# Performance work log

Measured on AMD Instinct MI355X. Metric: run time of the kernel, lower is better.

## Reference

```python
import jax, jax.numpy as jnp
import numpy as np

N, E, DIN, H, CHID, COUT, S = 20000, 320000, 128, 4, 64, 64, 32
EPS_BN = 1e-5


def setup_inputs() -> dict:
    key = jax.random.key(0)
    ks = jax.random.split(key, 20)
    g = lambda k, shp, s=0.1: jax.random.normal(k, shp, dtype=jnp.float32) * s
    return {
        "x": jax.random.normal(ks[0], (N, DIN), dtype=jnp.float32),
        "edge_index": jax.random.randint(ks[1], (2, E), 0, N, dtype=jnp.int32),
        "struct_feat": jax.random.normal(ks[2], (N, S), dtype=jnp.float32),
        # GATConv (layer 1)
        "W1": g(ks[3], (H * CHID, DIN)),
        "att_src1": g(ks[4], (1, H, CHID)),
        "att_dst1": g(ks[5], (1, H, CHID)),
        "bias1": jnp.zeros((CHID,), jnp.float32),
        # HybridGateGATLayer (layer 2)
        "W2": g(ks[6], (H * COUT, CHID)),
        "att_src2": g(ks[7], (1, H, COUT)),
        "att_dst2": g(ks[8], (1, H, COUT)),
        "bias2": jnp.zeros((COUT,), jnp.float32),
        "Wt": g(ks[9], (1, S)),
        "bt": jnp.zeros((1,), jnp.float32),
        "We1": g(ks[10], (8, 4), 0.5),
        "be1": jnp.zeros((8,), jnp.float32),
        "We2": g(ks[11], (1, 8), 0.5),
        "be2": jnp.zeros((1,), jnp.float32),
        "betas": jnp.array([1.15, 0.85, 0.1, 0.08, 0.12], jnp.float32),
    }


def _seg_softmax(logits, seg, n):
    m = jax.ops.segment_max(logits, seg, num_segments=n)
    m = jnp.where(jnp.isfinite(m), m, 0.0)
    ex = jnp.exp(logits - m[seg])
    s = jax.ops.segment_sum(ex, seg, num_segments=n)
    return ex / (s[seg] + 1e-16)


def _cos(a, b):
    na = jnp.maximum(jnp.linalg.norm(a, axis=-1), 1e-8)
    nb = jnp.maximum(jnp.linalg.norm(b, axis=-1), 1e-8)
    return (a * b).sum(-1) / (na * nb)


def reference(x, edge_index, struct_feat, W1, att_src1, att_dst1, bias1,
              W2, att_src2, att_dst2, bias2, Wt, bt, We1, be1, We2, be2, betas):
    n = x.shape[0]
    src0, dst0 = edge_index[0], edge_index[1]
    # ---- layer 1: standard GATConv with self loops, concat=False (head mean) ----
    loop = jnp.arange(n, dtype=src0.dtype)
    src = jnp.concatenate([src0, loop])
    dst = jnp.concatenate([dst0, loop])
    h = (x @ W1.T).reshape(n, H, CHID)
    a_s = (h * att_src1).sum(-1)  # [N,H]
    a_d = (h * att_dst1).sum(-1)
    al = jax.nn.leaky_relu(a_s[src] + a_d[dst], 0.2)  # [E+N,H]
    alpha1 = _seg_softmax(al, dst, n)
    out1 = jax.ops.segment_sum(h[src] * alpha1[..., None], dst, num_segments=n)
    h1 = jax.nn.relu(out1.mean(1) + bias1)  # [N,CHID]
    # batch norm (affine=False, batch stats, biased var)
    mu = h1.mean(0)
    var = ((h1 - mu) ** 2).mean(0)
    h1 = (h1 - mu) / jnp.sqrt(var + EPS_BN)
    # ---- layer 2: HybridGateGATLayer (no self loops) ----
    x2 = (h1 @ W2.T).reshape(n, H, COUT)
    node_trust = jax.nn.sigmoid(struct_feat @ Wt.T + bt).squeeze(-1)  # [N]
    as2 = (x2 * att_src2).sum(-1)
    ad2 = (x2 * att_dst2).sum(-1)
    j, i = src0, dst0
    alpha_raw = jax.nn.leaky_relu(as2[j] + ad2[i], 0.2)  # [E,H]
    struct_sim = _cos(struct_feat[j], struct_feat[i])  # [E]
    xf = x2.reshape(n, H * COUT)
    feat_sim = _cos(xf[j], xf[i])
    agreement = struct_sim * feat_sim
    conflict = jnp.abs(struct_sim - feat_sim)
    cues = jnp.stack([struct_sim, feat_sim, agreement, conflict], axis=-1)  # [E,4]
    gate = (jax.nn.relu(cues @ We1.T + be1) @ We2.T + be2).squeeze(-1)
    edge_bonus = jax.nn.sigmoid(gate) * jax.nn.relu(agreement)
    edge_trust = jnp.sqrt(jnp.clip(node_trust[j] * node_trust[i], 0.0))
    trust_bonus = edge_trust * jax.nn.relu(0.5 * (struct_sim + feat_sim))
    gate_logit = (betas[0] * struct_sim + betas[1] * feat_sim + betas[2] * agreement
                  + betas[3] * edge_bonus + betas[4] * trust_bonus)
    alpha2 = _seg_softmax(alpha_raw + gate_logit[:, None], i, n)  # [E,H]
    out2 = jax.ops.segment_sum(x2[j] * alpha2[..., None], i, num_segments=n)
    return out2.mean(1) + bias2  # [N,COUT]
```

## Files before the change

### kernel.cpp

```cpp
#include <hip/hip_runtime.h>
#include <hip/hip_bf16.h>
#include <hip/hip_fp16.h>

#define C_DIN 128
#define C_H 4
#define C_CH 64
#define C_HC 256
#define C_S 32
#define ACH 32
#define MBLK 64
#define XROW 264

typedef __attribute__((ext_vector_type(8))) _Float16 half8;
typedef __attribute__((ext_vector_type(4))) float f32x4;

__device__ __forceinline__ float lrelu(float x) { return x >= 0.f ? x : 0.2f * x; }

__device__ __forceinline__ float sub_sum32(float v) {
#pragma unroll
    for (int off = 16; off > 0; off >>= 1) v += __shfl_xor(v, off);
    return v;
}

__global__ void k_count(const int* __restrict__ dst, int* __restrict__ deg, int E) {
    int e = blockIdx.x * blockDim.x + threadIdx.x;
    if (e < E) atomicAdd(&deg[dst[e]], 1);
}

__global__ void k_scan(const int* __restrict__ deg, int* __restrict__ row_ptr,
                       int* __restrict__ cursor, int n) {
    __shared__ int part[1024];
    int t = threadIdx.x;
    const int C = (n + 1023) / 1024;
    int base = t * C;
    int s = 0;
    for (int k = 0; k < C; ++k) {
        int idx = base + k;
        if (idx < n) s += deg[idx];
    }
    part[t] = s;
    __syncthreads();
    for (int off = 1; off < 1024; off <<= 1) {
        int v = (t >= off) ? part[t - off] : 0;
        __syncthreads();
        part[t] += v;
        __syncthreads();
    }
    int run = (t == 0) ? 0 : part[t - 1];
    for (int k = 0; k < C; ++k) {
        int idx = base + k;
        if (idx < n) { row_ptr[idx] = run; cursor[idx] = run; run += deg[idx]; }
    }
    if (t == 1023) row_ptr[n] = run;
}

__global__ void k_scatter(const int* __restrict__ src, const int* __restrict__ dst,
                          int* __restrict__ cursor, int* __restrict__ adj_src, int E) {
    int e = blockIdx.x * blockDim.x + threadIdx.x;
    if (e < E) {
        int d = dst[e];
        int p = atomicAdd(&cursor[d], 1);
        adj_src[p] = src[e];
    }
}

__global__ void k_prepw(const float* __restrict__ W1, const float* __restrict__ W2,
                        _Float16* __restrict__ W1f, _Float16* __restrict__ W2f) {
    int i = blockIdx.x * blockDim.x + threadIdx.x;
    if (i < 4096) {
        int ks = i >> 10, rem = i & 1023, nt = rem >> 6, lpos = rem & 63;
        int c = nt * 16 + (lpos & 15);
        int kb = (ks * 4 + (lpos >> 4)) * 8;
        const float4* src = (const float4*)(W1 + (size_t)c * C_DIN + kb);
        float4 f0 = src[0], f1 = src[1];
        _Float16* dst = &W1f[(size_t)i * 8];
        dst[0] = (_Float16)f0.x; dst[1] = (_Float16)f0.y;
        dst[2] = (_Float16)f0.z; dst[3] = (_Float16)f0.w;
        dst[4] = (_Float16)f1.x; dst[5] = (_Float16)f1.y;
        dst[6] = (_Float16)f1.z; dst[7] = (_Float16)f1.w;
    } else if (i < 4096 + 2048) {
        int ii = i - 4096;
        int ks = ii >> 10, rem = ii & 1023, nt = rem >> 6, lpos = rem & 63;
        int c = nt * 16 + (lpos & 15);
        int kb = (ks * 4 + (lpos >> 4)) * 8;
        const float4* src = (const float4*)(W2 + (size_t)c * C_CH + kb);
        float4 f0 = src[0], f1 = src[1];
        _Float16* dst = &W2f[(size_t)ii * 8];
        dst[0] = (_Float16)f0.x; dst[1] = (_Float16)f0.y;
        dst[2] = (_Float16)f0.z; dst[3] = (_Float16)f0.w;
        dst[4] = (_Float16)f1.x; dst[5] = (_Float16)f1.y;
        dst[6] = (_Float16)f1.z; dst[7] = (_Float16)f1.w;
    }
}

__global__ __launch_bounds__(256) void k_gemm1(
    const float* __restrict__ x, const _Float16* __restrict__ W1f,
    const float* __restrict__ att_s, const float* __restrict__ att_d,
    __half* __restrict__ hh_out, float* __restrict__ a_s, float* __restrict__ a_d, int n) {
    __shared__ __align__(16) _Float16 as_[4 * 4 * 64 * 8];
    int t = threadIdx.x;
    int r0 = blockIdx.x * MBLK;
    {
        int row = t >> 2, q = t & 3;
        int rr = r0 + row;
        int mt = row >> 4, rl = row & 15;
        const float4* xrow = (const float4*)(x + (size_t)rr * C_DIN);
#pragma unroll
        for (int cc = 0; cc < 4; ++cc) {
            int ch = q * 4 + cc;
            float4 f0 = make_float4(0, 0, 0, 0), f1 = make_float4(0, 0, 0, 0);
            if (rr < n) { f0 = xrow[ch * 2]; f1 = xrow[ch * 2 + 1]; }
            int ks = ch >> 2, lg = ch & 3;
            _Float16* dst = &as_[(((ks * 4 + mt) * 64) + (lg * 16 + rl)) * 8];
            dst[0] = (_Float16)f0.x; dst[1] = (_Float16)f0.y;
            dst[2] = (_Float16)f0.z; dst[3] = (_Float16)f0.w;
            dst[4] = (_Float16)f1.x; dst[5] = (_Float16)f1.y;
            dst[6] = (_Float16)f1.z; dst[7] = (_Float16)f1.w;
        }
    }
    __syncthreads();
    int w = t >> 6, l = t & 63;
    const half8* Wv = (const half8*)W1f;
    f32x4 acc[4][4];
#pragma unroll
    for (int mt = 0; mt < 4; ++mt)
#pragma unroll
        for (int nt = 0; nt < 4; ++nt) acc[mt][nt] = (f32x4){0.f, 0.f, 0.f, 0.f};
#pragma unroll
    for (int ks = 0; ks < 4; ++ks) {
        half8 af[4], bf[4];
#pragma unroll
        for (int mt = 0; mt < 4; ++mt)
            af[mt] = *(const half8*)&as_[(((ks * 4 + mt) * 64) + l) * 8];
#pragma unroll
        for (int nt = 0; nt < 4; ++nt)
            bf[nt] = Wv[((ks * 16 + (w * 4 + nt)) * 64) + l];
#pragma unroll
        for (int mt = 0; mt < 4; ++mt)
#pragma unroll
            for (int nt = 0; nt < 4; ++nt)
                acc[mt][nt] = __builtin_amdgcn_mfma_f32_16x16x32_f16(af[mt], bf[nt],
                                                                     acc[mt][nt], 0, 0, 0);
    }
    int cl = l & 15, rg = l >> 4;
    float atv_s[4], atv_d[4];
#pragma unroll
    for (int nt = 0; nt < 4; ++nt) {
        atv_s[nt] = att_s[w * 64 + nt * 16 + cl];
        atv_d[nt] = att_d[w * 64 + nt * 16 + cl];
    }
#pragma unroll
    for (int mt = 0; mt < 4; ++mt) {
#pragma unroll
        for (int r = 0; r < 4; ++r) {
            int rr = r0 + mt * 16 + rg * 4 + r;
            float vs = 0.f, vd = 0.f;
#pragma unroll
            for (int nt = 0; nt < 4; ++nt) {
                float v = acc[mt][nt][r];
                vs += atv_s[nt] * v;
                vd += atv_d[nt] * v;
                if (rr < n)
                    hh_out[(size_t)rr * C_HC + w * 64 + nt * 16 + cl] = __float2half(v);
            }
#pragma unroll
            for (int off = 1; off < 16; off <<= 1) {
                vs += __shfl_xor(vs, off);
                vd += __shfl_xor(vd, off);
            }
            if (cl == 0 && rr < n) { a_s[rr * C_H + w] = vs; a_d[rr * C_H + w] = vd; }
        }
    }
}

__global__ void k_layer1(const int* __restrict__ row_ptr, const int* __restrict__ adj_src,
                         const __half* __restrict__ hhlf, const float* __restrict__ a_s,
                         const float* __restrict__ a_d, const float* __restrict__ bias1,
                         float* __restrict__ h1) {
    int d = blockIdx.x;
    int t = threadIdx.x, hh = t >> 5, cp = t & 31;
    int beg = row_ptr[d], end = row_ptr[d + 1];
    float adh = a_d[d * C_H + hh];
    float p_self = expf(lrelu(a_s[d * C_H + hh] + adh));
    __shared__ float alpha_l[C_H][ACH];
    __shared__ int src_l[ACH];
    const __half2* selfrow = (const __half2*)(hhlf + (size_t)d * C_HC + hh * 64);
    float2 sv = __half22float2(selfrow[cp]);
    float accx = p_self * sv.x, accy = p_self * sv.y;
    float s_part = (cp == 0) ? p_self : 0.f;
    for (int cbeg = beg; cbeg < end; cbeg += ACH) {
        int cn = min(end - cbeg, ACH);
        __syncthreads();
        if (cp < cn) {
            int s = adj_src[cbeg + cp];
            if (hh == 0) src_l[cp] = s;
            float p = expf(lrelu(a_s[s * C_H + hh] + adh));
            alpha_l[hh][cp] = p;
            s_part += p;
        }
        __syncthreads();
        for (int i = 0; i < cn; ++i) {
            int s = src_l[i];
            float a = alpha_l[hh][i];
            float2 v = __half22float2(
                *(const __half2*)(hhlf + (size_t)s * C_HC + hh * 64 + cp * 2));
            accx += a * v.x;
            accy += a * v.y;
        }
    }
    float s = sub_sum32(s_part);
    float inv = 1.f / (s + 1e-16f);
    __shared__ float2 red[128];
    red[t] = make_float2(accx * inv, accy * inv);
    __syncthreads();
    if (t < 32) {
        float2 r0 = red[t], r1 = red[t + 32], r2 = red[t + 64], r3 = red[t + 96];
        float2 b = *(const float2*)&bias1[t * 2];
        float vx = (r0.x + r1.x + r2.x + r3.x) * 0.25f + b.x;
        float vy = (r0.y + r1.y + r2.y + r3.y) * 0.25f + b.y;
        *(float2*)&h1[(size_t)d * C_CH + t * 2] =
            make_float2(fmaxf(vx, 0.f), fmaxf(vy, 0.f));
    }
}

__global__ void k_bnstats(const float* __restrict__ h1, float* __restrict__ bn, int n) {
    int t = threadIdx.x;
    int c = t & 63, rg = t >> 6;
    float s = 0.f, s2 = 0.f;
    for (int r = blockIdx.x * 4 + rg; r < n; r += gridDim.x * 4) {
        float v = h1[(size_t)r * C_CH + c];
        s += v;
        s2 += v * v;
    }
    __shared__ float ls[256], ls2[256];
    ls[t] = s; ls2[t] = s2;
    __syncthreads();
    if (t < 64) {
        s = ls[t] + ls[t + 64] + ls[t + 128] + ls[t + 192];
        s2 = ls2[t] + ls2[t + 64] + ls2[t + 128] + ls2[t + 192];
        atomicAdd(&bn[c], s);
        atomicAdd(&bn[64 + c], s2);
    }
}

__global__ __launch_bounds__(256) void k_gemm2(
    const float* __restrict__ h1, const _Float16* __restrict__ W2f,
    const float* __restrict__ att_s, const float* __restrict__ att_d,
    const float* __restrict__ bn, __half* __restrict__ x2h,
    float* __restrict__ as2, float* __restrict__ ad2, float* __restrict__ nf, int n) {
    __shared__ __align__(16) _Float16 as_[2 * 4 * 64 * 8];
    __shared__ float nq[64][4];
    int t = threadIdx.x;
    int r0 = blockIdx.x * MBLK;
    {
        int row = t >> 2, q = t & 3;
        int rr = r0 + row;
        int mt = row >> 4, rl = row & 15;
        const float invN = 1.f / (float)n;
        const float4* hrow = (const float4*)(h1 + (size_t)rr * C_CH);
#pragma unroll
        for (int cc = 0; cc < 2; ++cc) {
            int ch = q * 2 + cc;
            float4 f0 = make_float4(0, 0, 0, 0), f1 = make_float4(0, 0, 0, 0);
            if (rr < n) { f0 = hrow[ch * 2]; f1 = hrow[ch * 2 + 1]; }
            float4 s0 = *(const float4*)&bn[ch * 8];
            float4 s1 = *(const float4*)&bn[ch * 8 + 4];
            float4 q0 = *(const float4*)&bn[64 + ch * 8];
            float4 q1 = *(const float4*)&bn[64 + ch * 8 + 4];
            float4 mu0 = make_float4(s0.x * invN, s0.y * invN, s0.z * invN, s0.w * invN);
            float4 mu1 = make_float4(s1.x * invN, s1.y * invN, s1.z * invN, s1.w * invN);
            float4 rs0 = make_float4(rsqrtf(q0.x * invN - mu0.x * mu0.x + 1e-5f),
                                     rsqrtf(q0.y * invN - mu0.y * mu0.y + 1e-5f),
                                     rsqrtf(q0.z * invN - mu0.z * mu0.z + 1e-5f),
                                     rsqrtf(q0.w * invN - mu0.w * mu0.w + 1e-5f));
            float4 rs1 = make_float4(rsqrtf(q1.x * invN - mu1.x * mu1.x + 1e-5f),
                                     rsqrtf(q1.y * invN - mu1.y * mu1.y + 1e-5f),
                                     rsqrtf(q1.z * invN - mu1.z * mu1.z + 1e-5f),
                                     rsqrtf(q1.w * invN - mu1.w * mu1.w + 1e-5f));
            int ks = ch >> 2, lg = ch & 3;
            _Float16* dst = &as_[(((ks * 4 + mt) * 64) + (lg * 16 + rl)) * 8];
            dst[0] = (_Float16)((f0.x - mu0.x) * rs0.x);
            dst[1] = (_Float16)((f0.y - mu0.y) * rs0.y);
            dst[2] = (_Float16)((f0.z - mu0.z) * rs0.z);
            dst[3] = (_Float16)((f0.w - mu0.w) * rs0.w);
            dst[4] = (_Float16)((f1.x - mu1.x) * rs1.x);
            dst[5] = (_Float16)((f1.y - mu1.y) * rs1.y);
            dst[6] = (_Float16)((f1.z - mu1.z) * rs1.z);
            dst[7] = (_Float16)((f1.w - mu1.w) * rs1.w);
        }
    }
    __syncthreads();
    int w = t >> 6, l = t & 63;
    const half8* Wv = (const half8*)W2f;
    f32x4 acc[4][4];
#pragma unroll
    for (int mt = 0; mt < 4; ++mt)
#pragma unroll
        for (int nt = 0; nt < 4; ++nt) acc[mt][nt] = (f32x4){0.f, 0.f, 0.f, 0.f};
#pragma unroll
    for (int ks = 0; ks < 2; ++ks) {
        half8 af[4], bf[4];
#pragma unroll
        for (int mt = 0; mt < 4; ++mt)
            af[mt] = *(const half8*)&as_[(((ks * 4 + mt) * 64) + l) * 8];
#pragma unroll
        for (int nt = 0; nt < 4; ++nt)
            bf[nt] = Wv[((ks * 16 + (w * 4 + nt)) * 64) + l];
#pragma unroll
        for (int mt = 0; mt < 4; ++mt)
#pragma unroll
            for (int nt = 0; nt < 4; ++nt)
                acc[mt][nt] = __builtin_amdgcn_mfma_f32_16x16x32_f16(af[mt], bf[nt],
                                                                     acc[mt][nt], 0, 0, 0);
    }
    int cl = l & 15, rg = l >> 4;
    float atv_s[4], atv_d[4];
#pragma unroll
    for (int nt = 0; nt < 4; ++nt) {
        atv_s[nt] = att_s[w * 64 + nt * 16 + cl];
        atv_d[nt] = att_d[w * 64 + nt * 16 + cl];
    }
#pragma unroll
    for (int mt = 0; mt < 4; ++mt) {
#pragma unroll
        for (int r = 0; r < 4; ++r) {
            int rr = r0 + mt * 16 + rg * 4 + r;
            float vs = 0.f, vd = 0.f, vq = 0.f;
#pragma unroll
            for (int nt = 0; nt < 4; ++nt) {
                float v = acc[mt][nt][r];
                vs += atv_s[nt] * v;
                vd += atv_d[nt] * v;
                vq += v * v;
                if (rr < n)
                    x2h[(size_t)rr * C_HC + w * 64 + nt * 16 + cl] = __float2half(v);
            }
#pragma unroll
            for (int off = 1; off < 16; off <<= 1) {
                vs += __shfl_xor(vs, off);
                vd += __shfl_xor(vd, off);
                vq += __shfl_xor(vq, off);
            }
            if (cl == 0 && rr < n) {
                as2[rr * C_H + w] = vs;
                ad2[rr * C_H + w] = vd;
                nq[mt * 16 + rg * 4 + r][w] = vq;
            }
        }
    }
    __syncthreads();
    if (t < MBLK) {
        int rr = r0 + t;
        if (rr < n) {
            float qq = nq[t][0] + nq[t][1] + nq[t][2] + nq[t][3];
            nf[rr] = fmaxf(sqrtf(qq), 1e-8f);
        }
    }
}

__global__ void k_trust(const float* __restrict__ sf, const float* __restrict__ Wt,
                        const float* __restrict__ bt, float* __restrict__ trust,
                        float* __restrict__ ns, int n) {
    int i = blockIdx.x * blockDim.x + threadIdx.x;
    if (i >= n) return;
    const float4* r4 = (const float4*)(sf + (size_t)i * C_S);
    const float4* w4 = (const float4*)Wt;
    float d = 0.f, q = 0.f;
#pragma unroll
    for (int k = 0; k < 8; ++k) {
        float4 a = r4[k], w = w4[k];
        d += a.x * w.x + a.y * w.y + a.z * w.z + a.w * w.w;
        q += a.x * a.x + a.y * a.y + a.z * a.z + a.w * a.w;
    }
    trust[i] = 1.f / (1.f + expf(-(d + bt[0])));
    ns[i] = fmaxf(sqrtf(q), 1e-8f);
}

__global__ __launch_bounds__(128) void k_fused2(
    const int* __restrict__ row_ptr, const int* __restrict__ adj_src,
    const float* __restrict__ sf, const __half* __restrict__ x2h,
    const float* __restrict__ ns, const float* __restrict__ nf,
    const float* __restrict__ trust, const float* __restrict__ as2,
    const float* __restrict__ ad2, const float* __restrict__ We1,
    const float* __restrict__ be1, const float* __restrict__ We2,
    const float* __restrict__ be2, const float* __restrict__ betas,
    const float* __restrict__ bias2, float* __restrict__ out) {
    __shared__ __align__(16) _Float16 xr[ACH * XROW];
    __shared__ int js[ACH];
    __shared__ float fdL[ACH], sdL[ACH];
    __shared__ float pbuf[C_H][ACH];
    __shared__ float2 red[128];
    int d = blockIdx.x;
    int t = threadIdx.x, hh = t >> 5, cp = t & 31;
    int beg = row_ptr[d], end = row_ptr[d + 1];
    float4 xd4 = ((const float4*)(x2h + (size_t)d * C_HC))[cp];
    float sfdl = sf[(size_t)d * C_S + cp];
    float4 ad2d = *(const float4*)&ad2[d * C_H];
    float nsd = ns[d], nfd = nf[d], trd = trust[d];
    float accx = 0.f, accy = 0.f, s_part = 0.f;
    for (int cbeg = beg; cbeg < end; cbeg += ACH) {
        int cn = min(end - cbeg, ACH);
        __syncthreads();
        if (t < cn) js[t] = adj_src[cbeg + t];
        __syncthreads();
        for (int r = hh; r < cn; r += 4) {
            int j = js[r];
            float4 v4 = ((const float4*)(x2h + (size_t)j * C_HC))[cp];
            ((float4*)&xr[(size_t)r * XROW])[cp] = v4;
            float fdp = 0.f;
            const __half2* pa = (const __half2*)&v4;
            const __half2* pb = (const __half2*)&xd4;
#pragma unroll
            for (int k = 0; k < 4; ++k) {
                float2 a = __half22float2(pa[k]), b = __half22float2(pb[k]);
                fdp += a.x * b.x + a.y * b.y;
            }
            float sdp = sf[(size_t)j * C_S + cp] * sfdl;
#pragma unroll
            for (int off = 16; off > 0; off >>= 1) {
                fdp += __shfl_xor(fdp, off);
                sdp += __shfl_xor(sdp, off);
            }
            if (cp == 0) { fdL[r] = fdp; sdL[r] = sdp; }
        }
        __syncthreads();
        if (t < cn) {
            int j = js[t];
            float ss = sdL[t] / (nsd * ns[j]);
            float fs = fdL[t] / (nfd * nf[j]);
            float agr = ss * fs;
            float con = fabsf(ss - fs);
            float gate = be2[0];
#pragma unroll
            for (int o = 0; o < 8; ++o) {
                float hdn = We1[o * 4 + 0] * ss + We1[o * 4 + 1] * fs +
                            We1[o * 4 + 2] * agr + We1[o * 4 + 3] * con + be1[o];
                gate += We2[o] * fmaxf(hdn, 0.f);
            }
            float eb = (1.f / (1.f + expf(-gate))) * fmaxf(agr, 0.f);
            float et = sqrtf(fmaxf(trd * trust[j], 0.f));
            float tb = et * fmaxf(0.5f * (ss + fs), 0.f);
            float g = betas[0] * ss + betas[1] * fs + betas[2] * agr +
                      betas[3] * eb + betas[4] * tb;
            float4 asj = *(const float4*)&as2[j * C_H];
            pbuf[0][t] = expf(lrelu(asj.x + ad2d.x) + g);
            pbuf[1][t] = expf(lrelu(asj.y + ad2d.y) + g);
            pbuf[2][t] = expf(lrelu(asj.z + ad2d.z) + g);
            pbuf[3][t] = expf(lrelu(asj.w + ad2d.w) + g);
        }
        __syncthreads();
        for (int i = 0; i < cn; ++i) {
            float pv = pbuf[hh][i];
            float2 v = __half22float2(
                *(const __half2*)&xr[(size_t)i * XROW + hh * 64 + cp * 2]);
            accx += pv * v.x;
            accy += pv * v.y;
        }
        if (cp < cn) s_part += pbuf[hh][cp];
    }
    float s = sub_sum32(s_part);
    float inv = 1.f / (s + 1e-16f);
    red[t] = make_float2(accx * inv, accy * inv);
    __syncthreads();
    if (t < 32) {
        float2 r0 = red[t], r1 = red[t + 32], r2 = red[t + 64], r3 = red[t + 96];
        float2 b = *(const float2*)&bias2[t * 2];
        float vx = (r0.x + r1.x + r2.x + r3.x) * 0.25f + b.x;
        float vy = (r0.y + r1.y + r2.y + r3.y) * 0.25f + b.y;
        *(float2*)&out[(size_t)d * C_CH + t * 2] = make_float2(vx, vy);
    }
}

static inline size_t al256(size_t x) { return (x + 255) & ~(size_t)255; }

extern "C" void kernel_launch(void* const* d_in, const int* in_sizes, int n_in,
                              void* d_out, int out_size, void* d_ws, size_t ws_size,
                              hipStream_t stream) {
    const float* x      = (const float*)d_in[0];
    const int*   ei     = (const int*)d_in[1];
    const float* sf     = (const float*)d_in[2];
    const float* W1     = (const float*)d_in[3];
    const float* atts1  = (const float*)d_in[4];
    const float* attd1  = (const float*)d_in[5];
    const float* bias1  = (const float*)d_in[6];
    const float* W2     = (const float*)d_in[7];
    const float* atts2  = (const float*)d_in[8];
    const float* attd2  = (const float*)d_in[9];
    const float* bias2  = (const float*)d_in[10];
    const float* Wt     = (const float*)d_in[11];
    const float* bt     = (const float*)d_in[12];
    const float* We1    = (const float*)d_in[13];
    const float* be1    = (const float*)d_in[14];
    const float* We2    = (const float*)d_in[15];
    const float* be2    = (const float*)d_in[16];
    const float* betas  = (const float*)d_in[17];

    const int N = in_sizes[0] / C_DIN;
    const int E = in_sizes[1] / 2;
    const int* srcs = ei;
    const int* dsts = ei + E;

    char* p = (char*)d_ws;
    size_t off = 0;
    auto take = [&](size_t bytes) { char* r = p + off; off = al256(off + bytes); return r; };
    __half* hhlf  = (__half*)take((size_t)N * C_HC * 2);
    float* h1     = (float*)take((size_t)N * C_CH * 4);
    float* a_s1   = (float*)take((size_t)N * C_H * 4);
    float* a_d1   = (float*)take((size_t)N * C_H * 4);
    float* nf     = (float*)take((size_t)N * 4);
    float* ns     = (float*)take((size_t)N * 4);
    float* trust  = (float*)take((size_t)N * 4);
    int*   deg    = (int*)take((size_t)N * 4);
    int*   rowp   = (int*)take((size_t)(N + 1) * 4);
    int*   cursor = (int*)take((size_t)N * 4);
    int*   adj_s  = (int*)take((size_t)E * 4);
    _Float16* W1f = (_Float16*)take(4096 * 8 * 2);
    _Float16* W2f = (_Float16*)take(2048 * 8 * 2);
    float* bn     = (float*)take(128 * 4);
    (void)ws_size;
    __half* x2h = hhlf;
    float* as2  = a_s1;
    float* ad2  = a_d1;

    hipMemsetAsync(deg, 0, (size_t)N * 4, stream);
    hipMemsetAsync(bn, 0, 128 * 4, stream);

    k_prepw<<<24, 256, 0, stream>>>(W1, W2, W1f, W2f);
    k_count<<<(E + 255) / 256, 256, 0, stream>>>(dsts, deg, E);
    k_scan<<<1, 1024, 0, stream>>>(deg, rowp, cursor, N);
    k_scatter<<<(E + 255) / 256, 256, 0, stream>>>(srcs, dsts, cursor, adj_s, E);

    k_gemm1<<<(N + MBLK - 1) / MBLK, 256, 0, stream>>>(x, W1f, atts1, attd1, hhlf, a_s1,
                                                       a_d1, N);
    k_layer1<<<N, 128, 0, stream>>>(rowp, adj_s, hhlf, a_s1, a_d1, bias1, h1);
    k_bnstats<<<128, 256, 0, stream>>>(h1, bn, N);

    k_gemm2<<<(N + MBLK - 1) / MBLK, 256, 0, stream>>>(h1, W2f, atts2, attd2, bn, x2h,
                                                       as2, ad2, nf, N);
    k_trust<<<(N + 255) / 256, 256, 0, stream>>>(sf, Wt, bt, trust, ns, N);
    k_fused2<<<N, 128, 0, stream>>>(rowp, adj_s, sf, x2h, ns, nf, trust, as2, ad2,
                                    We1, be1, We2, be2, betas, bias2, (float*)d_out);
}
```

Baseline: 307.4 us.

## Process one destination node per wavefront in both aggregation kernels

Rewrites the layer-1 aggregation and the fused layer-2 edge-gating kernels so that each 64-lane wavefront handles one destination node, with four edges in flight at a time (16 lanes per edge). Each lane loads 16 fp16 channels and accumulates in registers, and cross-edge and cross-head reductions use shuffles. This removes the shared-memory staging, __syncthreads barriers and one-block-per-node launches. The cost is higher register pressure (16 accumulators per lane) and wasted lanes for nodes whose degree is not a multiple of four.

```diff
diff --git a/kernel.cpp b/kernel.cpp
--- a/kernel.cpp
+++ b/kernel.cpp
@@ -7,20 +7,12 @@
 #define C_CH 64
 #define C_HC 256
 #define C_S 32
-#define ACH 32
 #define MBLK 64
-#define XROW 264
 
 typedef __attribute__((ext_vector_type(8))) _Float16 half8;
 typedef __attribute__((ext_vector_type(4))) float f32x4;
 
 __device__ __forceinline__ float lrelu(float x) { return x >= 0.f ? x : 0.2f * x; }
-
-__device__ __forceinline__ float sub_sum32(float v) {
-#pragma unroll
-    for (int off = 16; off > 0; off >>= 1) v += __shfl_xor(v, off);
-    return v;
-}
 
 __global__ void k_count(const int* __restrict__ dst, int* __restrict__ deg, int E) {
     int e = blockIdx.x * blockDim.x + threadIdx.x;
@@ -173,53 +165,73 @@
     }
 }
 
-__global__ void k_layer1(const int* __restrict__ row_ptr, const int* __restrict__ adj_src,
-                         const __half* __restrict__ hhlf, const float* __restrict__ a_s,
-                         const float* __restrict__ a_d, const float* __restrict__ bias1,
-                         float* __restrict__ h1) {
-    int d = blockIdx.x;
-    int t = threadIdx.x, hh = t >> 5, cp = t & 31;
+__global__ __launch_bounds__(256) void k_layer1(
+    const int* __restrict__ row_ptr, const int* __restrict__ adj_src,
+    const __half* __restrict__ hhlf, const float* __restrict__ a_s,
+    const float* __restrict__ a_d, const float* __restrict__ bias1,
+    float* __restrict__ h1, int n) {
+    int wid = (blockIdx.x * blockDim.x + threadIdx.x) >> 6;
+    if (wid >= n) return;
+    int l = threadIdx.x & 63, g = l >> 4, q = l & 15, h = q >> 2;
+    int d = wid;
     int beg = row_ptr[d], end = row_ptr[d + 1];
-    float adh = a_d[d * C_H + hh];
-    float p_self = expf(lrelu(a_s[d * C_H + hh] + adh));
-    __shared__ float alpha_l[C_H][ACH];
-    __shared__ int src_l[ACH];
-    const __half2* selfrow = (const __half2*)(hhlf + (size_t)d * C_HC + hh * 64);
-    float2 sv = __half22float2(selfrow[cp]);
-    float accx = p_self * sv.x, accy = p_self * sv.y;
-    float s_part = (cp == 0) ? p_self : 0.f;
-    for (int cbeg = beg; cbeg < end; cbeg += ACH) {
-        int cn = min(end - cbeg, ACH);
-        __syncthreads();
-        if (cp < cn) {
-            int s = adj_src[cbeg + cp];
-            if (hh == 0) src_l[cp] = s;
-            float p = expf(lrelu(a_s[s * C_H + hh] + adh));
-            alpha_l[hh][cp] = p;
-            s_part += p;
-        }
-        __syncthreads();
-        for (int i = 0; i < cn; ++i) {
-            int s = src_l[i];
-            float a = alpha_l[hh][i];
-            float2 v = __half22float2(
-                *(const __half2*)(hhlf + (size_t)s * C_HC + hh * 64 + cp * 2));
-            accx += a * v.x;
-            accy += a * v.y;
-        }
-    }
-    float s = sub_sum32(s_part);
+    float adh = a_d[d * C_H + h];
+    const float4* drow = (const float4*)(hhlf + (size_t)d * C_HC + q * 16);
+    float4 d0 = drow[0], d1 = drow[1];
+    float acc[16];
+#pragma unroll
+    for (int i = 0; i < 16; ++i) acc[i] = 0.f;
+    float s = 0.f;
+    if (g == 0) {
+        float ps = expf(lrelu(a_s[d * C_H + h] + adh));
+        const __half2* pa = (const __half2*)&d0;
+        const __half2* pb = (const __half2*)&d1;
+#pragma unroll
+        for (int k = 0; k < 4; ++k) {
+            float2 a = __half22float2(pa[k]);
+            acc[k * 2] += ps * a.x; acc[k * 2 + 1] += ps * a.y;
+            float2 b = __half22float2(pb[k]);
+            acc[8 + k * 2] += ps * b.x; acc[8 + k * 2 + 1] += ps * b.y;
+        }
+        s += ps;
+    }
+    for (int cb = beg; cb < end; cb += 4) {
+        int e = cb + g;
+        bool act = e < end;
+        int j = act ? adj_src[e] : d;
+        const float4* jrow = (const float4*)(hhlf + (size_t)j * C_HC + q * 16);
+        float4 r0 = jrow[0], r1 = jrow[1];
+        float p = act ? expf(lrelu(a_s[j * C_H + h] + adh)) : 0.f;
+        const __half2* pa = (const __half2*)&r0;
+        const __half2* pb = (const __half2*)&r1;
+#pragma unroll
+        for (int k = 0; k < 4; ++k) {
+            float2 a = __half22float2(pa[k]);
+            acc[k * 2] += p * a.x; acc[k * 2 + 1] += p * a.y;
+            float2 b = __half22float2(pb[k]);
+            acc[8 + k * 2] += p * b.x; acc[8 + k * 2 + 1] += p * b.y;
+        }
+        s += p;
+    }
+#pragma unroll
+    for (int off = 16; off <= 32; off <<= 1) {
+#pragma unroll
+        for (int i = 0; i < 16; ++i) acc[i] += __shfl_xor(acc[i], off);
+        s += __shfl_xor(s, off);
+    }
     float inv = 1.f / (s + 1e-16f);
-    __shared__ float2 red[128];
-    red[t] = make_float2(accx * inv, accy * inv);
-    __syncthreads();
-    if (t < 32) {
-        float2 r0 = red[t], r1 = red[t + 32], r2 = red[t + 64], r3 = red[t + 96];
-        float2 b = *(const float2*)&bias1[t * 2];
-        float vx = (r0.x + r1.x + r2.x + r3.x) * 0.25f + b.x;
-        float vy = (r0.y + r1.y + r2.y + r3.y) * 0.25f + b.y;
-        *(float2*)&h1[(size_t)d * C_CH + t * 2] =
-            make_float2(fmaxf(vx, 0.f), fmaxf(vy, 0.f));
+#pragma unroll
+    for (int i = 0; i < 16; ++i) acc[i] *= inv;
+#pragma unroll
+    for (int off = 4; off <= 8; off <<= 1) {
+#pragma unroll
+        for (int i = 0; i < 16; ++i) acc[i] += __shfl_xor(acc[i], off);
+    }
+    if (l < 4) {
+#pragma unroll
+        for (int i = 0; i < 16; ++i)
+            h1[(size_t)d * C_CH + l * 16 + i] =
+                fmaxf(acc[i] * 0.25f + bias1[l * 16 + i], 0.f);
     }
 }
 
@@ -277,7 +289,8 @@
                                      rsqrtf(q1.y * invN - mu1.y * mu1.y + 1e-5f),
                                      rsqrtf(q1.z * invN - mu1.z * mu1.z + 1e-5f),
                                      rsqrtf(q1.w * invN - mu1.w * mu1.w + 1e-5f));
-            int ks = ch >> 2, lg = ch & 3;
+            int ks = ch >> 1, lg = ch & 1;
+            ks = ch >> 2; lg = ch & 3;
             _Float16* dst = &as_[(((ks * 4 + mt) * 64) + (lg * 16 + rl)) * 8];
             dst[0] = (_Float16)((f0.x - mu0.x) * rs0.x);
             dst[1] = (_Float16)((f0.y - mu0.y) * rs0.y);
@@ -376,7 +389,7 @@
     ns[i] = fmaxf(sqrtf(q), 1e-8f);
 }
 
-__global__ __launch_bounds__(128) void k_fused2(
+__global__ __launch_bounds__(256) void k_fused2(
     const int* __restrict__ row_ptr, const int* __restrict__ adj_src,
     const float* __restrict__ sf, const __half* __restrict__ x2h,
     const float* __restrict__ ns, const float* __restrict__ nf,
@@ -384,53 +397,60 @@
     const float* __restrict__ ad2, const float* __restrict__ We1,
     const float* __restrict__ be1, const float* __restrict__ We2,
     const float* __restrict__ be2, const float* __restrict__ betas,
-    const float* __restrict__ bias2, float* __restrict__ out) {
-    __shared__ __align__(16) _Float16 xr[ACH * XROW];
-    __shared__ int js[ACH];
-    __shared__ float fdL[ACH], sdL[ACH];
-    __shared__ float pbuf[C_H][ACH];
-    __shared__ float2 red[128];
-    int d = blockIdx.x;
-    int t = threadIdx.x, hh = t >> 5, cp = t & 31;
+    const float* __restrict__ bias2, float* __restrict__ out, int n) {
+    int wid = (blockIdx.x * blockDim.x + threadIdx.x) >> 6;
+    if (wid >= n) return;
+    int l = threadIdx.x & 63, g = l >> 4, q = l & 15, h = q >> 2;
+    int d = wid;
     int beg = row_ptr[d], end = row_ptr[d + 1];
-    float4 xd4 = ((const float4*)(x2h + (size_t)d * C_HC))[cp];
-    float sfdl = sf[(size_t)d * C_S + cp];
-    float4 ad2d = *(const float4*)&ad2[d * C_H];
+    const float4* drow = (const float4*)(x2h + (size_t)d * C_HC + q * 16);
+    float4 d0 = drow[0], d1 = drow[1];
+    float2 sfd = *(const float2*)(sf + (size_t)d * C_S + q * 2);
+    float ad2h = ad2[d * C_H + h];
     float nsd = ns[d], nfd = nf[d], trd = trust[d];
-    float accx = 0.f, accy = 0.f, s_part = 0.f;
-    for (int cbeg = beg; cbeg < end; cbeg += ACH) {
-        int cn = min(end - cbeg, ACH);
-        __syncthreads();
-        if (t < cn) js[t] = adj_src[cbeg + t];
-        __syncthreads();
-        for (int r = hh; r < cn; r += 4) {
-            int j = js[r];
-            float4 v4 = ((const float4*)(x2h + (size_t)j * C_HC))[cp];
-            ((float4*)&xr[(size_t)r * XROW])[cp] = v4;
-            float fdp = 0.f;
-            const __half2* pa = (const __half2*)&v4;
-            const __half2* pb = (const __half2*)&xd4;
+    float b20 = be2[0];
+    float bt0 = betas[0], bt1 = betas[1], bt2 = betas[2], bt3 = betas[3], bt4 = betas[4];
+    float acc[16];
+#pragma unroll
+    for (int i = 0; i < 16; ++i) acc[i] = 0.f;
+    float s = 0.f;
+    for (int cb = beg; cb < end; cb += 4) {
+        int e = cb + g;
+        bool act = e < end;
+        int j = act ? adj_src[e] : d;
+        const float4* jrow = (const float4*)(x2h + (size_t)j * C_HC + q * 16);
+        float4 r0 = jrow[0], r1 = jrow[1];
+        float2 sfj = *(const float2*)(sf + (size_t)j * C_S + q * 2);
+        float fd = 0.f;
+        {
+            const __half2* pa = (const __half2*)&r0;
+            const __half2* pb = (const __half2*)&d0;
 #pragma unroll
             for (int k = 0; k < 4; ++k) {
                 float2 a = __half22float2(pa[k]), b = __half22float2(pb[k]);
-                fdp += a.x * b.x + a.y * b.y;
-            }
-            float sdp = sf[(size_t)j * C_S + cp] * sfdl;
-#pragma unroll
-            for (int off = 16; off > 0; off >>= 1) {
-                fdp += __shfl_xor(fdp, off);
-                sdp += __shfl_xor(sdp, off);
-            }
-            if (cp == 0) { fdL[r] = fdp; sdL[r] = sdp; }
-        }
-        __syncthreads();
-        if (t < cn) {
-            int j = js[t];
-            float ss = sdL[t] / (nsd * ns[j]);
-            float fs = fdL[t] / (nfd * nf[j]);
+                fd += a.x * b.x + a.y * b.y;
+            }
+            const __half2* pc = (const __half2*)&r1;
+            const __half2* pd = (const __half2*)&d1;
+#pragma unroll
+            for (int k = 0; k < 4; ++k) {
+                float2 a = __half22float2(pc[k]), b = __half22float2(pd[k]);
+                fd += a.x * b.x + a.y * b.y;
+            }
+        }
+        float sd = sfj.x * sfd.x + sfj.y * sfd.y;
+#pragma unroll
+        for (int off = 1; off < 16; off <<= 1) {
+            fd += __shfl_xor(fd, off);
+            sd += __shfl_xor(sd, off);
+        }
+        float p = 0.f;
+        if (act) {
+            float ss = sd / (nsd * ns[j]);
+            float fs = fd / (nfd * nf[j]);
             float agr = ss * fs;
             float con = fabsf(ss - fs);
-            float gate = be2[0];
+            float gate = b20;
 #pragma unroll
             for (int o = 0; o < 8; ++o) {
                 float hdn = We1[o * 4 + 0] * ss + We1[o * 4 + 1] * fs +
@@ -440,34 +460,40 @@
             float eb = (1.f / (1.f + expf(-gate))) * fmaxf(agr, 0.f);
             float et = sqrtf(fmaxf(trd * trust[j], 0.f));
             float tb = et * fmaxf(0.5f * (ss + fs), 0.f);
-            float g = betas[0] * ss + betas[1] * fs + betas[2] * agr +
-                      betas[3] * eb + betas[4] * tb;
-            float4 asj = *(const float4*)&as2[j * C_H];
-            pbuf[0][t] = expf(lrelu(asj.x + ad2d.x) + g);
-            pbuf[1][t] = expf(lrelu(asj.y + ad2d.y) + g);
-            pbuf[2][t] = expf(lrelu(asj.z + ad2d.z) + g);
-            pbuf[3][t] = expf(lrelu(asj.w + ad2d.w) + g);
-        }
-        __syncthreads();
-        for (int i = 0; i < cn; ++i) {
-            float pv = pbuf[hh][i];
-            float2 v = __half22float2(
-                *(const __half2*)&xr[(size_t)i * XROW + hh * 64 + cp * 2]);
-            accx += pv * v.x;
-            accy += pv * v.y;
-        }
-        if (cp < cn) s_part += pbuf[hh][cp];
-    }
-    float s = sub_sum32(s_part);
+            float glog = bt0 * ss + bt1 * fs + bt2 * agr + bt3 * eb + bt4 * tb;
+            p = expf(lrelu(as2[j * C_H + h] + ad2h) + glog);
+        }
+        {
+            const __half2* pa = (const __half2*)&r0;
+            const __half2* pb = (const __half2*)&r1;
+#pragma unroll
+            for (int k = 0; k < 4; ++k) {
+                float2 a = __half22float2(pa[k]);
+                acc[k * 2] += p * a.x; acc[k * 2 + 1] += p * a.y;
+                float2 b = __half22float2(pb[k]);
+                acc[8 + k * 2] += p * b.x; acc[8 + k * 2 + 1] += p * b.y;
+            }
+        }
+        s += p;
+    }
+#pragma unroll
+    for (int off = 16; off <= 32; off <<= 1) {
+#pragma unroll
+        for (int i = 0; i < 16; ++i) acc[i] += __shfl_xor(acc[i], off);
+        s += __shfl_xor(s, off);
+    }
     float inv = 1.f / (s + 1e-16f);
-    red[t] = make_float2(accx * inv, accy * inv);
-    __syncthreads();
-    if (t < 32) {
-        float2 r0 = red[t], r1 = red[t + 32], r2 = red[t + 64], r3 = red[t + 96];
-        float2 b = *(const float2*)&bias2[t * 2];
-        float vx = (r0.x + r1.x + r2.x + r3.x) * 0.25f + b.x;
-        float vy = (r0.y + r1.y + r2.y + r3.y) * 0.25f + b.y;
-        *(float2*)&out[(size_t)d * C_CH + t * 2] = make_float2(vx, vy);
+#pragma unroll
+    for (int i = 0; i < 16; ++i) acc[i] *= inv;
+#pragma unroll
+    for (int off = 4; off <= 8; off <<= 1) {
+#pragma unroll
+        for (int i = 0; i < 16; ++i) acc[i] += __shfl_xor(acc[i], off);
+    }
+    if (l < 4) {
+#pragma unroll
+        for (int i = 0; i < 16; ++i)
+            out[(size_t)d * C_CH + l * 16 + i] = acc[i] * 0.25f + bias2[l * 16 + i];
     }
 }
 
@@ -532,12 +558,13 @@
 
     k_gemm1<<<(N + MBLK - 1) / MBLK, 256, 0, stream>>>(x, W1f, atts1, attd1, hhlf, a_s1,
                                                        a_d1, N);
-    k_layer1<<<N, 128, 0, stream>>>(rowp, adj_s, hhlf, a_s1, a_d1, bias1, h1);
+    k_layer1<<<(N + 3) / 4, 256, 0, stream>>>(rowp, adj_s, hhlf, a_s1, a_d1, bias1, h1, N);
     k_bnstats<<<128, 256, 0, stream>>>(h1, bn, N);
 
     k_gemm2<<<(N + MBLK - 1) / MBLK, 256, 0, stream>>>(h1, W2f, atts2, attd2, bn, x2h,
                                                        as2, ad2, nf, N);
     k_trust<<<(N + 255) / 256, 256, 0, stream>>>(sf, Wt, bt, trust, ns, N);
-    k_fused2<<<N, 128, 0, stream>>>(rowp, adj_s, sf, x2h, ns, nf, trust, as2, ad2,
-                                    We1, be1, We2, be2, betas, bias2, (float*)d_out);
-}
+    k_fused2<<<(N + 3) / 4, 256, 0, stream>>>(rowp, adj_s, sf, x2h, ns, nf, trust, as2, ad2,
+                                              We1, be1, We2, be2, betas, bias2,
+                                              (float*)d_out, N);
+}
```

Result: no change. 306.8 us (-0.2%).
